# Kernel tuning notes

Measured on AMD Instinct MI355X. Metric: run time of the kernel, lower is better.

Reference implementation:

```python
import jax, jax.numpy as jnp
import numpy as np

B = 64       # number of graphs (regular batching)
NPER = 2048  # nodes per graph
K = 16       # kNN neighbors (includes self, as torch_cluster.knn does)
D_IN = 64
D_OUT = 64


def setup_inputs() -> dict:
    key = jax.random.key(0)
    k1, k2 = jax.random.split(key, 2)
    x = jax.random.normal(k1, (B * NPER, D_IN), jnp.float32)
    batch = jnp.repeat(jnp.arange(B, dtype=jnp.int32), NPER)
    # MLP: Linear(2*in_channels, out_channels, bias=True) + ReLU
    weight = jax.random.normal(k2, (D_OUT, 2 * D_IN), jnp.float32) * (1.0 / np.sqrt(2 * D_IN))
    bias = jnp.zeros((D_OUT,), jnp.float32)
    return {"x": x, "batch": batch, "weight": weight, "bias": bias}


def reference(x, batch, weight, bias):
    # batch is a regular assignment (NPER nodes per graph) -> block the kNN per graph
    d = x.shape[1]
    xb = x.reshape(B, NPER, d)                                   # [B, n, d]
    # squared euclidean distances within each graph
    sq = jnp.sum(xb * xb, axis=-1)                               # [B, n]
    dist = sq[:, :, None] + sq[:, None, :] - 2.0 * jnp.einsum('bnd,bmd->bnm', xb, xb)
    # k nearest (smallest distance); self-distance 0 -> self included, matching PyG knn
    _, idx = jax.lax.top_k(-dist, K)                             # [B, n, K]
    xj = jax.vmap(lambda feats, ids: feats[ids])(xb, idx)        # [B, n, K, d]
    xi = xb[:, :, None, :]                                        # [B, n, 1, d]
    msg = jnp.concatenate([jnp.broadcast_to(xi, xj.shape), xj - xi], axis=-1)  # [B,n,K,2d]
    h = jax.nn.relu(jnp.einsum('bnkf,of->bnko', msg, weight) + bias)
    out = jnp.max(h, axis=2)                                      # max aggregation over neighbors
    return out.reshape(B * NPER, -1)
```

## Files before the change

### kernel.cpp

```cpp
#include <hip/hip_runtime.h>
#include <cfloat>

#define BB 64
#define NPERB 2048
#define KNN 16
#define NTOT (BB*NPERB)
#define NCAND 24

typedef __bf16 bf16x8 __attribute__((ext_vector_type(8)));
typedef float  f32x4  __attribute__((ext_vector_type(4)));

__device__ __forceinline__ unsigned int med3u(unsigned int a, unsigned int b, unsigned int c) {
    unsigned int d;
    asm("v_med3_u32 %0, %1, %2, %3" : "=v"(d) : "v"(a), "v"(b), "v"(c));
    return d;
}

__device__ __forceinline__ float np_sq64(const float* __restrict__ xs) {
    float r[8];
#pragma unroll
    for (int j = 0; j < 8; ++j) r[j] = __fmul_rn(xs[j], xs[j]);
#pragma unroll
    for (int i = 1; i < 8; ++i)
#pragma unroll
        for (int j = 0; j < 8; ++j)
            r[j] = __fadd_rn(r[j], __fmul_rn(xs[8*i + j], xs[8*i + j]));
    float t01 = __fadd_rn(r[0], r[1]);
    float t23 = __fadd_rn(r[2], r[3]);
    float t45 = __fadd_rn(r[4], r[5]);
    float t67 = __fadd_rn(r[6], r[7]);
    return __fadd_rn(__fadd_rn(t01, t23), __fadd_rn(t45, t67));
}

__device__ __forceinline__ unsigned short bf16rn(float f) {
    unsigned int u = __float_as_uint(f);
    u += 0x7fffu + ((u >> 16) & 1u);
    return (unsigned short)(u >> 16);
}
__device__ __forceinline__ unsigned int pk2(float a, float b) {
    return ((unsigned int)bf16rn(b) << 16) | (unsigned int)bf16rn(a);
}

__global__ __launch_bounds__(256) void k_transform(const float* __restrict__ x,
    const float* __restrict__ w, const float* __restrict__ bias,
    float* __restrict__ Aout, float* __restrict__ Bvv, float* __restrict__ sqnp,
    unsigned int* __restrict__ xbu)
{
    __shared__ float w1m[64*64];
    __shared__ float w2t[64*64];
    __shared__ float xs[128*64];
    int t = threadIdx.x;
    int r0 = blockIdx.x * 128;
#pragma unroll
    for (int i = 0; i < 16; ++i) {
        int e = t + i*256; int f = e >> 6; int o = e & 63;
        float w2 = w[o*128 + 64 + f];
        float w1 = w[o*128 + f];
        w2t[f*64 + o] = w2;
        w1m[f*64 + o] = w1 - w2;
    }
#pragma unroll
    for (int i = 0; i < 32; ++i) { int idx = t + i*256; xs[idx] = x[(size_t)r0*64 + idx]; }
    __syncthreads();
#pragma unroll
    for (int i = 0; i < 16; ++i) {
        int e = t + i*256;
        xbu[(size_t)r0*32 + e] = pk2(xs[2*e], xs[2*e + 1]);
    }
    int o = t & 63;
    float br = bias[o];
    for (int g = 0; g < 32; ++g) {
        int rl = g*4 + (t >> 6);
        float a1 = 0.f, a2 = 0.f;
#pragma unroll
        for (int f = 0; f < 64; ++f) {
            float xv = xs[rl*64 + f];
            a1 += xv * w1m[f*64 + o];
            a2 += xv * w2t[f*64 + o];
        }
        int row = r0 + rl;
        Aout[(size_t)row*64 + o] = a1 + br;
        Bvv[(size_t)row*64 + o] = a2;
        if (o == 0) sqnp[row] = np_sq64(&xs[rl*64]);
    }
}

__global__ __launch_bounds__(256, 4) void k_topk(const float4* __restrict__ x4,
    const uint4* __restrict__ xb, const float* __restrict__ sq, int* __restrict__ nbr)
{
    __shared__ __align__(16) char smem[28160];
    unsigned short* bsh0 = (unsigned short*)smem;
    unsigned short* bsh1 = (unsigned short*)(smem + 9216);
    unsigned short* rsh  = (unsigned short*)(smem + 18432);
    float* sqc           = (float*)(smem + 27648);
    unsigned int* cand   = (unsigned int*)smem;
    unsigned short* cand24 = (unsigned short*)(smem + 17408);

    int t = threadIdx.x;
    int lane = t & 63;
    int w = t >> 6;
    int ln = lane & 15, qd = lane >> 4;
    int batch = blockIdx.x >> 5;
    int strip = blockIdx.x & 31;
    int rbase = batch * NPERB;
    int r0g = rbase + strip * 64;

    {
        const uint4* src = xb + (size_t)r0g * 8;
#pragma unroll
        for (int i = 0; i < 2; ++i) {
            int l = t + i*256;
            uint4 v = src[l];
            *(uint4*)&rsh[(l >> 3)*72 + (l & 7)*8] = v;
        }
    }
    uint4 pf0, pf1; float sqpf;
    {
        const uint4* src = xb + (size_t)rbase * 8;
        pf0 = src[t]; pf1 = src[t + 256];
        sqpf = (t < 64) ? sq[rbase + t] : 0.f;
    }
    __syncthreads();
    bf16x8 rf0 = *(const bf16x8*)&rsh[(w*16 + ln)*72 + qd*8];
    bf16x8 rf1 = *(const bf16x8*)&rsh[(w*16 + ln)*72 + 32 + qd*8];
    float sqr16 = sq[r0g + w*16 + ln] + 16.f;

    *(uint4*)&bsh0[(t >> 3)*72 + (t & 7)*8] = pf0;
    { int l1 = t + 256; *(uint4*)&bsh0[(l1 >> 3)*72 + (l1 & 7)*8] = pf1; }
    if (t < 64) sqc[t] = sqpf;
    {
        const uint4* src = xb + ((size_t)rbase + 64) * 8;
        pf0 = src[t]; pf1 = src[t + 256];
        sqpf = (t < 64) ? sq[rbase + 64 + t] : 0.f;
    }
    __syncthreads();

    unsigned int ks[16];
#pragma unroll
    for (int j = 0; j < 16; ++j) ks[j] = 0xFFFFFFFFu;

    for (int ct = 0; ct < 32; ++ct) {
        unsigned short* bcur = (ct & 1) ? bsh1 : bsh0;
        const float* sqcur = sqc + (ct & 1)*64;
#pragma unroll
        for (int ct2 = 0; ct2 < 4; ++ct2) {
            int pt = ct2*16 + ln;
            bf16x8 a0 = *(const bf16x8*)&bcur[pt*72 + qd*8];
            bf16x8 a1 = *(const bf16x8*)&bcur[pt*72 + 32 + qd*8];
            f32x4 acc = {0.f, 0.f, 0.f, 0.f};
            acc = __builtin_amdgcn_mfma_f32_16x16x32_bf16(a0, rf0, acc, 0, 0, 0);
            acc = __builtin_amdgcn_mfma_f32_16x16x32_bf16(a1, rf1, acc, 0, 0, 0);
            f32x4 sc4 = *(const f32x4*)&sqcur[ct2*16 + qd*4];
            int idxb = ct*64 + ct2*16 + qd*4;
#pragma unroll
            for (int j = 0; j < 4; ++j) {
                float s = fmaf(-2.f, acc[j], sc4[j] + sqr16);
                unsigned int u = (__float_as_uint(s) & 0xFFFFF800u) | (unsigned int)(idxb + j);
#pragma unroll
                for (int jj = 15; jj >= 1; --jj) ks[jj] = med3u(u, ks[jj-1], ks[jj]);
                ks[0] = min(ks[0], u);
            }
        }
        if (ct < 31) {
            unsigned short* bnext = (ct & 1) ? bsh0 : bsh1;
            *(uint4*)&bnext[(t >> 3)*72 + (t & 7)*8] = pf0;
            { int l1 = t + 256; *(uint4*)&bnext[(l1 >> 3)*72 + (l1 & 7)*8] = pf1; }
            if (t < 64) sqc[((ct + 1) & 1)*64 + t] = sqpf;
            if (ct < 30) {
                const uint4* src = xb + ((size_t)rbase + (ct + 2)*64) * 8;
                pf0 = src[t]; pf1 = src[t + 256];
                sqpf = (t < 64) ? sq[rbase + (ct + 2)*64 + t] : 0.f;
            }
        }
        __syncthreads();
    }

    {
        int r = w*16 + ln;
#pragma unroll
        for (int j = 0; j < 16; ++j) cand[r*68 + qd*16 + j] = ks[j];
    }
    __syncthreads();

    if (t < 64) {
        unsigned int m24[NCAND];
#pragma unroll
        for (int j = 0; j < NCAND; ++j) m24[j] = 0xFFFFFFFFu;
        for (int i = 0; i < 64; ++i) {
            unsigned int u = cand[t*68 + i];
#pragma unroll
            for (int jj = NCAND-1; jj >= 1; --jj) m24[jj] = med3u(u, m24[jj-1], m24[jj]);
            m24[0] = min(m24[0], u);
        }
#pragma unroll
        for (int j = 0; j < NCAND; ++j) cand24[t*NCAND + j] = (unsigned short)(m24[j] & 0x7FFu);
    }
    __syncthreads();

    {
        int r = t & 63, grp = t >> 6;
        float sqr = sq[r0g + r];
        float4 xrA[8];
#pragma unroll
        for (int i = 0; i < 8; ++i) xrA[i] = x4[(size_t)(r0g + r)*16 + i];
        float* kdf = (float*)cand;
#pragma unroll
        for (int m6 = 0; m6 < 6; ++m6) {
            int m = grp*6 + m6;
            int c = (int)cand24[r*NCAND + m];
            const float4* xb4 = &x4[(size_t)(rbase + c)*16];
            float dot = 0.f;
#pragma unroll
            for (int i = 0; i < 8; ++i) {
                float4 a = xrA[i]; float4 b = xb4[i];
                dot = fmaf(a.x, b.x, dot); dot = fmaf(a.y, b.y, dot);
                dot = fmaf(a.z, b.z, dot); dot = fmaf(a.w, b.w, dot);
            }
#pragma unroll
            for (int i = 8; i < 16; ++i) {
                float4 a = x4[(size_t)(r0g + r)*16 + i]; float4 b = xb4[i];
                dot = fmaf(a.x, b.x, dot); dot = fmaf(a.y, b.y, dot);
                dot = fmaf(a.z, b.z, dot); dot = fmaf(a.w, b.w, dot);
            }
            float kd = __fsub_rn(__fadd_rn(sqr, sq[rbase + c]), __fmul_rn(2.0f, dot));
            kdf[r*68 + m] = kd;
            cand[r*68 + 32 + m] = (unsigned int)c;
        }
    }
    __syncthreads();

    if (t < 64) {
        float* kdf = (float*)cand;
        float dk[KNN]; int di[KNN];
#pragma unroll
        for (int j = 0; j < KNN; ++j) { dk[j] = FLT_MAX; di[j] = 0x7fffffff; }
        for (int m = 0; m < NCAND; ++m) {
            float kd = kdf[t*68 + m];
            int c = (int)cand[t*68 + 32 + m];
            bool better = (kd < dk[KNN-1]) || (kd == dk[KNN-1] && c < di[KNN-1]);
            if (better) {
#pragma unroll
                for (int j = KNN-1; j >= 1; --j) {
                    bool sh = (dk[j-1] > kd) || (dk[j-1] == kd && di[j-1] > c);
                    bool pl = (!sh) && ((dk[j] > kd) || (dk[j] == kd && di[j] > c));
                    float nk = sh ? dk[j-1] : (pl ? kd : dk[j]);
                    int ni = sh ? di[j-1] : (pl ? c : di[j]);
                    dk[j] = nk; di[j] = ni;
                }
                if ((dk[0] > kd) || (dk[0] == kd && di[0] > c)) { dk[0] = kd; di[0] = c; }
            }
        }
#pragma unroll
        for (int k = 0; k < KNN; ++k) nbr[(size_t)(r0g + t)*16 + k] = di[k];
    }
}

__global__ __launch_bounds__(256) void k_combine(const float* __restrict__ Bvv,
    const int* __restrict__ nbr, float* __restrict__ out)
{
    int t = threadIdx.x;
    int row = blockIdx.x*4 + (t >> 6);
    int o = t & 63;
    int rb = (row >> 11) << 11;
    float m = -FLT_MAX;
#pragma unroll
    for (int k = 0; k < 16; ++k) {
        int c = nbr[(size_t)row*16 + k];
        m = fmaxf(m, Bvv[(size_t)(rb + c)*64 + o]);
    }
    out[(size_t)row*64 + o] = fmaxf(out[(size_t)row*64 + o] + m, 0.f);
}

extern "C" void kernel_launch(void* const* d_in, const int* in_sizes, int n_in,
                              void* d_out, int out_size, void* d_ws, size_t ws_size,
                              hipStream_t stream) {
    const float* x    = (const float*)d_in[0];
    const float* w    = (const float*)d_in[2];
    const float* bias = (const float*)d_in[3];
    float* out = (float*)d_out;

    float* Bvv  = (float*)d_ws;
    float* sqnp = Bvv + (size_t)NTOT * 64;
    int*   nbr  = (int*)(sqnp + NTOT);
    unsigned int* xbu = (unsigned int*)(nbr + (size_t)NTOT * 16);

    k_transform<<<1024, 256, 0, stream>>>(x, w, bias, out, Bvv, sqnp, xbu);
    k_topk<<<2048, 256, 0, stream>>>((const float4*)x, (const uint4*)xbu, sqnp, nbr);
    k_combine<<<NTOT/4, 256, 0, stream>>>(Bvv, nbr, out);
}
```

Before: 635.2 us.

## Rewrite transform as one-row-per-thread and shrink top-k shared memory

The transform kernel now assigns one row per thread and holds its 64 features in registers. Weights are read straight from global/L1 with uniform addresses instead of being staged in shared memory, and outputs are written as float4. The top-k kernel reuses the row-staging buffer as the first candidate tile, which cuts shared memory from about 28KB to 20KB. It adds a barrier for that reuse and raises the launch-bounds occupancy hint from 4 to 8 blocks. The risks are register pressure in both kernels, possible spills under the tighter launch bound, and uncoalesced per-thread row loads in the transform.

```diff
diff --git a/kernel.cpp b/kernel.cpp
--- a/kernel.cpp
+++ b/kernel.cpp
@@ -16,22 +16,6 @@
     return d;
 }
 
-__device__ __forceinline__ float np_sq64(const float* __restrict__ xs) {
-    float r[8];
-#pragma unroll
-    for (int j = 0; j < 8; ++j) r[j] = __fmul_rn(xs[j], xs[j]);
-#pragma unroll
-    for (int i = 1; i < 8; ++i)
-#pragma unroll
-        for (int j = 0; j < 8; ++j)
-            r[j] = __fadd_rn(r[j], __fmul_rn(xs[8*i + j], xs[8*i + j]));
-    float t01 = __fadd_rn(r[0], r[1]);
-    float t23 = __fadd_rn(r[2], r[3]);
-    float t45 = __fadd_rn(r[4], r[5]);
-    float t67 = __fadd_rn(r[6], r[7]);
-    return __fadd_rn(__fadd_rn(t01, t23), __fadd_rn(t45, t67));
-}
-
 __device__ __forceinline__ unsigned short bf16rn(float f) {
     unsigned int u = __float_as_uint(f);
     u += 0x7fffu + ((u >> 16) & 1u);
@@ -41,58 +25,75 @@
     return ((unsigned int)bf16rn(b) << 16) | (unsigned int)bf16rn(a);
 }
 
-__global__ __launch_bounds__(256) void k_transform(const float* __restrict__ x,
+__global__ __launch_bounds__(256) void k_transform(const float4* __restrict__ x4,
     const float* __restrict__ w, const float* __restrict__ bias,
     float* __restrict__ Aout, float* __restrict__ Bvv, float* __restrict__ sqnp,
-    unsigned int* __restrict__ xbu)
+    uint4* __restrict__ xbu4)
 {
-    __shared__ float w1m[64*64];
-    __shared__ float w2t[64*64];
-    __shared__ float xs[128*64];
-    int t = threadIdx.x;
-    int r0 = blockIdx.x * 128;
-#pragma unroll
-    for (int i = 0; i < 16; ++i) {
-        int e = t + i*256; int f = e >> 6; int o = e & 63;
-        float w2 = w[o*128 + 64 + f];
-        float w1 = w[o*128 + f];
-        w2t[f*64 + o] = w2;
-        w1m[f*64 + o] = w1 - w2;
-    }
-#pragma unroll
-    for (int i = 0; i < 32; ++i) { int idx = t + i*256; xs[idx] = x[(size_t)r0*64 + idx]; }
-    __syncthreads();
-#pragma unroll
-    for (int i = 0; i < 16; ++i) {
-        int e = t + i*256;
-        xbu[(size_t)r0*32 + e] = pk2(xs[2*e], xs[2*e + 1]);
-    }
-    int o = t & 63;
-    float br = bias[o];
-    for (int g = 0; g < 32; ++g) {
-        int rl = g*4 + (t >> 6);
-        float a1 = 0.f, a2 = 0.f;
-#pragma unroll
-        for (int f = 0; f < 64; ++f) {
-            float xv = xs[rl*64 + f];
-            a1 += xv * w1m[f*64 + o];
-            a2 += xv * w2t[f*64 + o];
-        }
-        int row = r0 + rl;
-        Aout[(size_t)row*64 + o] = a1 + br;
-        Bvv[(size_t)row*64 + o] = a2;
-        if (o == 0) sqnp[row] = np_sq64(&xs[rl*64]);
-    }
-}
-
-__global__ __launch_bounds__(256, 4) void k_topk(const float4* __restrict__ x4,
+    const int r = blockIdx.x * 256 + threadIdx.x;
+    float xr[64];
+#pragma unroll
+    for (int j = 0; j < 16; ++j) {
+        float4 v = x4[(size_t)r * 16 + j];
+        xr[4*j+0] = v.x; xr[4*j+1] = v.y; xr[4*j+2] = v.z; xr[4*j+3] = v.w;
+    }
+
+    {
+        float rr[8];
+#pragma unroll
+        for (int j = 0; j < 8; ++j) rr[j] = __fmul_rn(xr[j], xr[j]);
+#pragma unroll
+        for (int i = 1; i < 8; ++i)
+#pragma unroll
+            for (int j = 0; j < 8; ++j)
+                rr[j] = __fadd_rn(rr[j], __fmul_rn(xr[8*i + j], xr[8*i + j]));
+        float t01 = __fadd_rn(rr[0], rr[1]);
+        float t23 = __fadd_rn(rr[2], rr[3]);
+        float t45 = __fadd_rn(rr[4], rr[5]);
+        float t67 = __fadd_rn(rr[6], rr[7]);
+        sqnp[r] = __fadd_rn(__fadd_rn(t01, t23), __fadd_rn(t45, t67));
+    }
+
+#pragma unroll
+    for (int i = 0; i < 8; ++i) {
+        uint4 u;
+        u.x = pk2(xr[8*i+0], xr[8*i+1]);
+        u.y = pk2(xr[8*i+2], xr[8*i+3]);
+        u.z = pk2(xr[8*i+4], xr[8*i+5]);
+        u.w = pk2(xr[8*i+6], xr[8*i+7]);
+        xbu4[(size_t)r * 8 + i] = u;
+    }
+
+    for (int o = 0; o < 64; o += 4) {
+        float a4[4], b4[4];
+#pragma unroll
+        for (int oo = 0; oo < 4; ++oo) {
+            const float* wr = w + (size_t)(o + oo) * 128;
+            float a1 = 0.f, a2 = 0.f;
+#pragma unroll
+            for (int f = 0; f < 64; ++f) {
+                float xv  = xr[f];
+                float w2v = wr[64 + f];
+                float w1m = __fsub_rn(wr[f], w2v);
+                a1 = __builtin_fmaf(xv, w1m, a1);
+                a2 = __builtin_fmaf(xv, w2v, a2);
+            }
+            a4[oo] = __fadd_rn(a1, bias[o + oo]);
+            b4[oo] = a2;
+        }
+        *(float4*)&Aout[(size_t)r * 64 + o] = make_float4(a4[0], a4[1], a4[2], a4[3]);
+        *(float4*)&Bvv [(size_t)r * 64 + o] = make_float4(b4[0], b4[1], b4[2], b4[3]);
+    }
+}
+
+__global__ __launch_bounds__(256, 8) void k_topk(const float4* __restrict__ x4,
     const uint4* __restrict__ xb, const float* __restrict__ sq, int* __restrict__ nbr)
 {
-    __shared__ __align__(16) char smem[28160];
+    __shared__ __align__(16) char smem[20480];
     unsigned short* bsh0 = (unsigned short*)smem;
     unsigned short* bsh1 = (unsigned short*)(smem + 9216);
-    unsigned short* rsh  = (unsigned short*)(smem + 18432);
-    float* sqc           = (float*)(smem + 27648);
+    unsigned short* rsh  = (unsigned short*)smem;
+    float* sqc           = (float*)(smem + 18432);
     unsigned int* cand   = (unsigned int*)smem;
     unsigned short* cand24 = (unsigned short*)(smem + 17408);
 
@@ -124,6 +125,7 @@
     bf16x8 rf0 = *(const bf16x8*)&rsh[(w*16 + ln)*72 + qd*8];
     bf16x8 rf1 = *(const bf16x8*)&rsh[(w*16 + ln)*72 + 32 + qd*8];
     float sqr16 = sq[r0g + w*16 + ln] + 16.f;
+    __syncthreads();
 
     *(uint4*)&bsh0[(t >> 3)*72 + (t & 7)*8] = pf0;
     { int l1 = t + 256; *(uint4*)&bsh0[(l1 >> 3)*72 + (l1 & 7)*8] = pf1; }
@@ -284,7 +286,7 @@
     int*   nbr  = (int*)(sqnp + NTOT);
     unsigned int* xbu = (unsigned int*)(nbr + (size_t)NTOT * 16);
 
-    k_transform<<<1024, 256, 0, stream>>>(x, w, bias, out, Bvv, sqnp, xbu);
+    k_transform<<<NTOT/256, 256, 0, stream>>>((const float4*)x, w, bias, out, Bvv, sqnp, (uint4*)xbu);
     k_topk<<<2048, 256, 0, stream>>>((const float4*)x, (const uint4*)xbu, sqnp, nbr);
     k_combine<<<NTOT/4, 256, 0, stream>>>(Bvv, nbr, out);
 }
```

New measurement: 856.8 us. 1.35x slower.
